# Optimization experiments

Hardware: AMD Instinct MI355X
Metric: run time of the kernel (lower is better)

## Reference

```python
import jax, jax.numpy as jnp
import numpy as np

B, D, M = 1024, 4096, 128          # batch, input_dim, output_dim (num modules)
HS = [32, 64, 128, 256, 512]       # hidden_dims


def setup_inputs() -> dict:
    key = jax.random.key(0)
    ks = jax.random.split(key, 12)
    inp = {}
    inp["x"] = jax.random.normal(ks[0], (B, D), dtype=jnp.float32)
    # first dense layer: Linear(input_dim, hidden_dims[0]*output_dim)
    inp["W0"] = jax.random.normal(ks[1], (HS[0] * M, D), dtype=jnp.float32) / np.float32(np.sqrt(D))
    inp["b0"] = jnp.zeros((HS[0] * M,), jnp.float32)
    # block-diagonal MaskedLinear layers stored as per-module blocks [M, h_out, h_in]
    for i in range(len(HS) - 1):
        inp[f"W{i+1}"] = jax.random.normal(ks[2 + i], (M, HS[i + 1], HS[i]), dtype=jnp.float32) / np.float32(np.sqrt(HS[i]))
        inp[f"b{i+1}"] = jnp.zeros((M, HS[i + 1]), jnp.float32)
    # output MaskedLinear(h_last, 1, M): blocks [M, 1, h_last] stored as [M, h_last]
    inp["Wout"] = jax.random.normal(ks[10], (M, HS[-1]), dtype=jnp.float32) / np.float32(np.sqrt(HS[-1]))
    inp["bout"] = jnp.zeros((M,), jnp.float32)
    return inp


def reference(x, W0, b0, W1, b1, W2, b2, W3, b3, W4, b4, Wout, bout):
    # Dropout is inference-disabled; MaskedLinear's block-diagonal dense GEMM is
    # computed exactly as a grouped GEMM over the M module blocks (same math,
    # skipping the structurally-zero off-diagonal blocks).
    h = jax.nn.relu(x @ W0.T + b0)                 # [B, M*h0]
    h = h.reshape(x.shape[0], M, HS[0])            # [B, M, h0]
    for W, b in ((W1, b1), (W2, b2), (W3, b3), (W4, b4)):
        h = jax.nn.relu(jnp.einsum('bmi,moi->bmo', h, W) + b)  # [B, M, h_out]
    logits = jnp.einsum('bmi,mi->bm', h, Wout) + bout          # [B, M]
    return jax.nn.sigmoid(logits)
```

## Files before the change

### kernel.cpp

```cpp
#include <hip/hip_runtime.h>
#include <hip/hip_bf16.h>


using bf16 = __hip_bfloat16;
typedef short bf16x8 __attribute__((ext_vector_type(8)));
typedef float f32x4 __attribute__((ext_vector_type(4)));

constexpr int B_ = 1024;
constexpr int M_ = 128;

__device__ __forceinline__ void gload16_lds(const bf16* gp, bf16* lp) {
    __builtin_amdgcn_global_load_lds(
        (__attribute__((address_space(1))) void*)const_cast<bf16*>(gp),
        (__attribute__((address_space(3))) void*)lp,
        16, 0, 0);
}

struct CvtArgs {
    const float4* src[6];
    short4* dst[6];
};
__global__ void cvt_all(CvtArgs a) {
    constexpr int starts[7] = {0, 1048576, 5242880, 5308416, 5570560,
                               6619136, 10813440};
    int i = blockIdx.x * blockDim.x + threadIdx.x;
    if (i >= starts[6]) return;
    int s = 0;
#pragma unroll
    for (int k = 1; k < 6; ++k) s += (i >= starts[k]) ? 1 : 0;
    int off = i - starts[s];
    float4 v = a.src[s][off];
    union { bf16 h[4]; short4 s4; } u;
    u.h[0] = __float2bfloat16(v.x);
    u.h[1] = __float2bfloat16(v.y);
    u.h[2] = __float2bfloat16(v.z);
    u.h[3] = __float2bfloat16(v.w);
    a.dst[s][off] = u.s4;
}

template<int BM, int BN>
__global__ __launch_bounds__(256)
void gemm_bt_relu(const bf16* __restrict__ A, int lda,
                  const bf16* __restrict__ W,
                  const float* __restrict__ bias,
                  bf16* __restrict__ C, int ldc,
                  int K) {
    constexpr int BK = 32;
    constexpr int WM = BM / 2, WN = BN / 2;
    constexpr int TM = WM / 16, TN = WN / 16;
    constexpr int A_W = BM / 64;
    constexpr int B_W = BN / 64;

    __shared__ __align__(16) bf16 sA[BM][BK];
    __shared__ __align__(16) bf16 sB[BN][BK];

    const int tid = threadIdx.x;
    const int wid = tid >> 6;
    const int lane = tid & 63;
    const int wm = wid >> 1, wn = wid & 1;
    const int q = lane >> 4, ln = lane & 15;
    const int lr = lane >> 2, lk = lane & 3;

    const int r0 = blockIdx.y * BM;
    const int c0 = blockIdx.x * BN;

    const bf16* gA[A_W];
    bf16* lA[A_W];
#pragma unroll
    for (int t = 0; t < A_W; ++t) {
        int grp = wid * A_W + t;
        gA[t] = A + (size_t)(r0 + grp * 16 + lr) * lda + lk * 8;
        lA[t] = &sA[grp * 16][0];
    }
    const bf16* gB[B_W];
    bf16* lB[B_W];
#pragma unroll
    for (int t = 0; t < B_W; ++t) {
        int grp = wid * B_W + t;
        gB[t] = W + (size_t)(c0 + grp * 16 + lr) * K + lk * 8;
        lB[t] = &sB[grp * 16][0];
    }

    f32x4 acc[TM][TN];
#pragma unroll
    for (int i = 0; i < TM; ++i)
#pragma unroll
        for (int j = 0; j < TN; ++j)
            acc[i][j] = (f32x4){0.f, 0.f, 0.f, 0.f};

    for (int k0 = 0; k0 < K; k0 += BK) {
#pragma unroll
        for (int t = 0; t < A_W; ++t) gload16_lds(gA[t] + k0, lA[t]);
#pragma unroll
        for (int t = 0; t < B_W; ++t) gload16_lds(gB[t] + k0, lB[t]);
        __syncthreads();

        bf16x8 aF[TM], bF[TN];
#pragma unroll
        for (int i = 0; i < TM; ++i)
            aF[i] = *(const bf16x8*)&sA[wm * WM + i * 16 + ln][q * 8];
#pragma unroll
        for (int j = 0; j < TN; ++j)
            bF[j] = *(const bf16x8*)&sB[wn * WN + j * 16 + ln][q * 8];
#pragma unroll
        for (int i = 0; i < TM; ++i)
#pragma unroll
            for (int j = 0; j < TN; ++j)
                acc[i][j] = __builtin_amdgcn_mfma_f32_16x16x32_bf16(aF[i], bF[j], acc[i][j], 0, 0, 0);
        __syncthreads();
    }

#pragma unroll
    for (int j = 0; j < TN; ++j) {
        int col = c0 + wn * WN + j * 16 + ln;
        float bv = bias[col];
#pragma unroll
        for (int i = 0; i < TM; ++i) {
#pragma unroll
            for (int r = 0; r < 4; ++r) {
                int row = r0 + wm * WM + i * 16 + q * 4 + r;
                float v = acc[i][j][r] + bv;
                v = v > 0.f ? v : 0.f;
                C[(size_t)row * ldc + col] = __float2bfloat16(v);
            }
        }
    }
}

__global__ __launch_bounds__(256)
void modules_fused(const bf16* __restrict__ h0g,
                   const bf16* __restrict__ W1b, const float* __restrict__ b1,
                   const bf16* __restrict__ W2b, const float* __restrict__ b2,
                   const bf16* __restrict__ W3b, const float* __restrict__ b3,
                   const bf16* __restrict__ W4b, const float* __restrict__ b4,
                   const float* __restrict__ Wout, const float* __restrict__ bout,
                   float* __restrict__ out) {
    constexpr int H3O = 0, H2O = 16384, H1O = 24576, H0O = 28672;
    constexpr int W1O = 30720, W2O = 28672, W3O = 24576, W4O = 16384;
    __shared__ __align__(16) bf16 pool[32768];

    const int tid = threadIdx.x, w = tid >> 6, lane = tid & 63;
    const int q = lane >> 4, ln = lane & 15;
    const int lr = lane >> 2, lk = lane & 3;
    const int swz = (lk ^ (lr & 3)) * 8;
    const int m = blockIdx.y;
    const int r0 = blockIdx.x * 64;

    const bf16* W1m = W1b + (size_t)m * 64 * 32;
    const bf16* W2m = W2b + (size_t)m * 128 * 64;
    const bf16* W3m = W3b + (size_t)m * 256 * 128;
    const bf16* W4m = W4b + (size_t)m * 512 * 256;

    auto stageW = [&](const bf16* G, int ldg, int rows, int nr0, int k0, int woff) {
        for (int t = 0; t < rows / 64; ++t) {
            int r = t * 64 + w * 16 + lr;
            gload16_lds(G + (size_t)(nr0 + r) * ldg + k0 + swz,
                        pool + woff + t * 2048 + w * 512);
        }
    };
    auto readA = [&](int hoff, int C, int row, int kc) -> bf16x8 {
        return *(const bf16x8*)&pool[hoff + row * (C * 8) + ((kc ^ (row & (C - 1))) * 8)];
    };
    auto readB = [&](int woff, int rn) -> bf16x8 {
        return *(const bf16x8*)&pool[woff + rn * 32 + ((q ^ (rn & 3)) * 8)];
    };
    auto writeH = [&](int hoff, int C, int row, int col, float v) {
        pool[hoff + row * (C * 8) + (((col >> 3) ^ (row & (C - 1))) * 8) + (col & 7)] =
            __float2bfloat16(v);
    };

    gload16_lds(h0g + (size_t)(r0 + w * 16 + lr) * 4096 + m * 32 + swz,
                pool + H0O + w * 512);
    stageW(W1m, 32, 64, 0, 0, W1O);
    __syncthreads();
    {
        f32x4 a1[4];
#pragma unroll
        for (int i = 0; i < 4; ++i) a1[i] = (f32x4){0.f, 0.f, 0.f, 0.f};
        bf16x8 bfr = readB(W1O, w * 16 + ln);
#pragma unroll
        for (int i = 0; i < 4; ++i) {
            bf16x8 af = readA(H0O, 4, i * 16 + ln, q);
            a1[i] = __builtin_amdgcn_mfma_f32_16x16x32_bf16(af, bfr, a1[i], 0, 0, 0);
        }
        int col = w * 16 + ln;
        float bb = b1[m * 64 + col];
#pragma unroll
        for (int i = 0; i < 4; ++i)
#pragma unroll
            for (int r = 0; r < 4; ++r) {
                float v = a1[i][r] + bb;
                v = v > 0.f ? v : 0.f;
                writeH(H1O, 8, i * 16 + q * 4 + r, col, v);
            }
    }
    __syncthreads();

    {
        f32x4 a2[4][2];
#pragma unroll
        for (int i = 0; i < 4; ++i)
#pragma unroll
            for (int j = 0; j < 2; ++j) a2[i][j] = (f32x4){0.f, 0.f, 0.f, 0.f};
#pragma unroll
        for (int kr = 0; kr < 2; ++kr) {
            stageW(W2m, 64, 128, 0, kr * 32, W2O);
            __syncthreads();
            bf16x8 bfr[2];
#pragma unroll
            for (int j = 0; j < 2; ++j) bfr[j] = readB(W2O, w * 32 + j * 16 + ln);
#pragma unroll
            for (int i = 0; i < 4; ++i) {
                bf16x8 af = readA(H1O, 8, i * 16 + ln, kr * 4 + q);
#pragma unroll
                for (int j = 0; j < 2; ++j)
                    a2[i][j] = __builtin_amdgcn_mfma_f32_16x16x32_bf16(af, bfr[j], a2[i][j], 0, 0, 0);
            }
            __syncthreads();
        }
#pragma unroll
        for (int j = 0; j < 2; ++j) {
            int col = w * 32 + j * 16 + ln;
            float bb = b2[m * 128 + col];
#pragma unroll
            for (int i = 0; i < 4; ++i)
#pragma unroll
                for (int r = 0; r < 4; ++r) {
                    float v = a2[i][j][r] + bb;
                    v = v > 0.f ? v : 0.f;
                    writeH(H2O, 16, i * 16 + q * 4 + r, col, v);
                }
        }
    }
    __syncthreads();

    {
        f32x4 a3[4][4];
#pragma unroll
        for (int i = 0; i < 4; ++i)
#pragma unroll
            for (int j = 0; j < 4; ++j) a3[i][j] = (f32x4){0.f, 0.f, 0.f, 0.f};
#pragma unroll
        for (int kr = 0; kr < 4; ++kr) {
            stageW(W3m, 128, 256, 0, kr * 32, W3O);
            __syncthreads();
            bf16x8 bfr[4];
#pragma unroll
            for (int j = 0; j < 4; ++j) bfr[j] = readB(W3O, w * 64 + j * 16 + ln);
#pragma unroll
            for (int i = 0; i < 4; ++i) {
                bf16x8 af = readA(H2O, 16, i * 16 + ln, kr * 4 + q);
#pragma unroll
                for (int j = 0; j < 4; ++j)
                    a3[i][j] = __builtin_amdgcn_mfma_f32_16x16x32_bf16(af, bfr[j], a3[i][j], 0, 0, 0);
            }
            __syncthreads();
        }
#pragma unroll
        for (int j = 0; j < 4; ++j) {
            int col = w * 64 + j * 16 + ln;
            float bb = b3[m * 256 + col];
#pragma unroll
            for (int i = 0; i < 4; ++i)
#pragma unroll
                for (int r = 0; r < 4; ++r) {
                    float v = a3[i][j][r] + bb;
                    v = v > 0.f ? v : 0.f;
                    writeH(H3O, 32, i * 16 + q * 4 + r, col, v);
                }
        }
    }
    __syncthreads();

    float pl[4][4];
#pragma unroll
    for (int i = 0; i < 4; ++i)
#pragma unroll
        for (int r = 0; r < 4; ++r) pl[i][r] = 0.f;

#pragma unroll
    for (int nc = 0; nc < 2; ++nc) {
        f32x4 a4[4][4];
#pragma unroll
        for (int i = 0; i < 4; ++i)
#pragma unroll
            for (int j = 0; j < 4; ++j) a4[i][j] = (f32x4){0.f, 0.f, 0.f, 0.f};
#pragma unroll
        for (int kr = 0; kr < 8; ++kr) {
            stageW(W4m, 256, 256, nc * 256, kr * 32, W4O);
            __syncthreads();
            bf16x8 bfr[4];
#pragma unroll
            for (int j = 0; j < 4; ++j) bfr[j] = readB(W4O, w * 64 + j * 16 + ln);
#pragma unroll
            for (int i = 0; i < 4; ++i) {
                bf16x8 af = readA(H3O, 32, i * 16 + ln, kr * 4 + q);
#pragma unroll
                for (int j = 0; j < 4; ++j)
                    a4[i][j] = __builtin_amdgcn_mfma_f32_16x16x32_bf16(af, bfr[j], a4[i][j], 0, 0, 0);
            }
            __syncthreads();
        }
#pragma unroll
        for (int j = 0; j < 4; ++j) {
            int col = nc * 256 + w * 64 + j * 16 + ln;
            float bb = b4[m * 512 + col];
            float wv = Wout[m * 512 + col];
#pragma unroll
            for (int i = 0; i < 4; ++i)
#pragma unroll
                for (int r = 0; r < 4; ++r) {
                    float v = a4[i][j][r] + bb;
                    v = v > 0.f ? v : 0.f;
                    pl[i][r] += v * wv;
                }
        }
    }

    float* sc = (float*)&pool[W4O];
#pragma unroll
    for (int i = 0; i < 4; ++i)
#pragma unroll
        for (int r = 0; r < 4; ++r) {
            float p = pl[i][r];
            p += __shfl_xor(p, 1);
            p += __shfl_xor(p, 2);
            p += __shfl_xor(p, 4);
            p += __shfl_xor(p, 8);
            if (ln == 0) sc[w * 64 + i * 16 + q * 4 + r] = p;
        }
    __syncthreads();
    if (tid < 64) {
        float s = sc[tid] + sc[64 + tid] + sc[128 + tid] + sc[192 + tid];
        float lg = s + bout[m];
        out[(size_t)(r0 + tid) * M_ + m] = 1.f / (1.f + __expf(-lg));
    }
}

extern "C" void kernel_launch(void* const* d_in, const int* in_sizes, int n_in,
                              void* d_out, int out_size, void* d_ws, size_t ws_size,
                              hipStream_t stream) {
    const float* x    = (const float*)d_in[0];
    const float* W0   = (const float*)d_in[1];
    const float* b0   = (const float*)d_in[2];
    const float* W1   = (const float*)d_in[3];
    const float* b1   = (const float*)d_in[4];
    const float* W2   = (const float*)d_in[5];
    const float* b2   = (const float*)d_in[6];
    const float* W3   = (const float*)d_in[7];
    const float* b3   = (const float*)d_in[8];
    const float* W4   = (const float*)d_in[9];
    const float* b4   = (const float*)d_in[10];
    const float* Wout = (const float*)d_in[11];
    const float* bout = (const float*)d_in[12];
    float* out = (float*)d_out;

    char* ws = (char*)d_ws;
    size_t off = 0;
    auto alloc = [&](size_t bytes) -> void* {
        off = (off + 255) & ~(size_t)255;
        void* p = ws + off;
        off += bytes;
        return p;
    };
    bf16* W0b = (bf16*)alloc((size_t)4096 * 4096 * 2);
    bf16* W1b = (bf16*)alloc((size_t)M_ * 64 * 32 * 2);
    bf16* W2b = (bf16*)alloc((size_t)M_ * 128 * 64 * 2);
    bf16* W3b = (bf16*)alloc((size_t)M_ * 256 * 128 * 2);
    bf16* W4b = (bf16*)alloc((size_t)M_ * 512 * 256 * 2);
    bf16* xb  = (bf16*)alloc((size_t)B_ * 4096 * 2);
    bf16* h0  = (bf16*)alloc((size_t)B_ * 4096 * 2);

    CvtArgs ca;
    ca.src[0] = (const float4*)x;  ca.dst[0] = (short4*)xb;
    ca.src[1] = (const float4*)W0; ca.dst[1] = (short4*)W0b;
    ca.src[2] = (const float4*)W1; ca.dst[2] = (short4*)W1b;
    ca.src[3] = (const float4*)W2; ca.dst[3] = (short4*)W2b;
    ca.src[4] = (const float4*)W3; ca.dst[4] = (short4*)W3b;
    ca.src[5] = (const float4*)W4; ca.dst[5] = (short4*)W4b;
    cvt_all<<<(10813440 + 255) / 256, 256, 0, stream>>>(ca);

    {
        dim3 g(4096 / 64, B_ / 128, 1);
        gemm_bt_relu<128, 64><<<g, 256, 0, stream>>>(xb, 4096, W0b, b0, h0, 4096, 4096);
    }
    {
        dim3 g(B_ / 64, M_, 1);
        modules_fused<<<g, 256, 0, stream>>>(h0, W1b, b1, W2b, b2, W3b, b3,
                                             W4b, b4, Wout, bout, out);
    }
}
```

Baseline: 356.7 us.

## Software-pipeline both GEMM kernels with multi-buffered async LDS loads

Replaces the generic layer-0 GEMM with a specialized kernel that double-buffers K=64 chunks, uses XOR-swizzled LDS layout, and overlaps global->LDS loads with MFMA using explicit vmcnt waits and barriers. The fused module kernel is likewise restructured: weight tiles for the next layer are prefetched during the current layer, layer 4 uses a triple-buffered 128-column pipeline, activations switch to padded row strides instead of XOR swizzles, and biases/Wout are preloaded into registers. The goal is to hide global load latency that the earlier load-sync-compute loops exposed. Hand-counted waitcnt values and occupancy hints of 2 blocks per CU add correctness and register-pressure risk.

```diff
diff --git a/kernel.cpp b/kernel.cpp
--- a/kernel.cpp
+++ b/kernel.cpp
@@ -8,6 +8,10 @@
 
 constexpr int B_ = 1024;
 constexpr int M_ = 128;
+
+#define WAITV(N) asm volatile("s_waitcnt vmcnt(" #N ")" ::: "memory")
+#define WAITL()  asm volatile("s_waitcnt lgkmcnt(0)" ::: "memory")
+#define BAR()    asm volatile("s_barrier" ::: "memory")
 
 __device__ __forceinline__ void gload16_lds(const bf16* gp, bf16* lp) {
     __builtin_amdgcn_global_load_lds(
@@ -38,96 +42,91 @@
     a.dst[s][off] = u.s4;
 }
 
-template<int BM, int BN>
-__global__ __launch_bounds__(256)
-void gemm_bt_relu(const bf16* __restrict__ A, int lda,
-                  const bf16* __restrict__ W,
-                  const float* __restrict__ bias,
-                  bf16* __restrict__ C, int ldc,
-                  int K) {
-    constexpr int BK = 32;
-    constexpr int WM = BM / 2, WN = BN / 2;
-    constexpr int TM = WM / 16, TN = WN / 16;
-    constexpr int A_W = BM / 64;
-    constexpr int B_W = BN / 64;
-
-    __shared__ __align__(16) bf16 sA[BM][BK];
-    __shared__ __align__(16) bf16 sB[BN][BK];
-
-    const int tid = threadIdx.x;
-    const int wid = tid >> 6;
-    const int lane = tid & 63;
-    const int wm = wid >> 1, wn = wid & 1;
+__global__ __launch_bounds__(256, 2)
+void gemm_l0(const bf16* __restrict__ A, const bf16* __restrict__ W,
+             const float* __restrict__ bias, bf16* __restrict__ C) {
+    constexpr int LDA = 4096;
+    __shared__ __align__(16) bf16 sA[2][2][128 * 32];
+    __shared__ __align__(16) bf16 sB[2][2][64 * 32];
+
+    const int tid = threadIdx.x, w = tid >> 6, lane = tid & 63;
     const int q = lane >> 4, ln = lane & 15;
     const int lr = lane >> 2, lk = lane & 3;
-
-    const int r0 = blockIdx.y * BM;
-    const int c0 = blockIdx.x * BN;
-
-    const bf16* gA[A_W];
-    bf16* lA[A_W];
-#pragma unroll
-    for (int t = 0; t < A_W; ++t) {
-        int grp = wid * A_W + t;
-        gA[t] = A + (size_t)(r0 + grp * 16 + lr) * lda + lk * 8;
-        lA[t] = &sA[grp * 16][0];
-    }
-    const bf16* gB[B_W];
-    bf16* lB[B_W];
-#pragma unroll
-    for (int t = 0; t < B_W; ++t) {
-        int grp = wid * B_W + t;
-        gB[t] = W + (size_t)(c0 + grp * 16 + lr) * K + lk * 8;
-        lB[t] = &sB[grp * 16][0];
-    }
-
-    f32x4 acc[TM][TN];
-#pragma unroll
-    for (int i = 0; i < TM; ++i)
-#pragma unroll
-        for (int j = 0; j < TN; ++j)
-            acc[i][j] = (f32x4){0.f, 0.f, 0.f, 0.f};
-
-    for (int k0 = 0; k0 < K; k0 += BK) {
-#pragma unroll
-        for (int t = 0; t < A_W; ++t) gload16_lds(gA[t] + k0, lA[t]);
-#pragma unroll
-        for (int t = 0; t < B_W; ++t) gload16_lds(gB[t] + k0, lB[t]);
-        __syncthreads();
-
-        bf16x8 aF[TM], bF[TN];
-#pragma unroll
-        for (int i = 0; i < TM; ++i)
-            aF[i] = *(const bf16x8*)&sA[wm * WM + i * 16 + ln][q * 8];
-#pragma unroll
-        for (int j = 0; j < TN; ++j)
-            bF[j] = *(const bf16x8*)&sB[wn * WN + j * 16 + ln][q * 8];
-#pragma unroll
-        for (int i = 0; i < TM; ++i)
-#pragma unroll
-            for (int j = 0; j < TN; ++j)
-                acc[i][j] = __builtin_amdgcn_mfma_f32_16x16x32_bf16(aF[i], bF[j], acc[i][j], 0, 0, 0);
-        __syncthreads();
-    }
-
-#pragma unroll
-    for (int j = 0; j < TN; ++j) {
-        int col = c0 + wn * WN + j * 16 + ln;
+    const int swz = (lk ^ (lr & 3)) * 8;
+    const int wm = w >> 1, wn = w & 1;
+    const int r0 = blockIdx.y * 128, c0 = blockIdx.x * 64;
+
+    auto stage = [&](int s, int set) {
+        const int k0 = s * 64;
+#pragma unroll
+        for (int h = 0; h < 2; ++h) {
+#pragma unroll
+            for (int t = 0; t < 2; ++t) {
+                int grp = w * 2 + t;
+                gload16_lds(A + (size_t)(r0 + grp * 16 + lr) * LDA + k0 + h * 32 + swz,
+                            &sA[set][h][grp * 512]);
+            }
+            gload16_lds(W + (size_t)(c0 + w * 16 + lr) * LDA + k0 + h * 32 + swz,
+                        &sB[set][h][w * 512]);
+        }
+    };
+
+    f32x4 acc[4][2];
+#pragma unroll
+    for (int i = 0; i < 4; ++i)
+#pragma unroll
+        for (int j = 0; j < 2; ++j) acc[i][j] = (f32x4){0.f, 0.f, 0.f, 0.f};
+
+    stage(0, 0);
+    stage(1, 1);
+    for (int r = 0; r < 64; ++r) {
+        if (r < 63) WAITV(6); else WAITV(0);
+        BAR();
+        const int set = r & 1;
+        bf16x8 aF[2][4], bF[2][2];
+#pragma unroll
+        for (int h = 0; h < 2; ++h) {
+#pragma unroll
+            for (int i = 0; i < 4; ++i) {
+                int row = wm * 64 + i * 16 + ln;
+                aF[h][i] = *(const bf16x8*)&sA[set][h][row * 32 + ((q ^ (row & 3)) * 8)];
+            }
+#pragma unroll
+            for (int j = 0; j < 2; ++j) {
+                int rn = wn * 32 + j * 16 + ln;
+                bF[h][j] = *(const bf16x8*)&sB[set][h][rn * 32 + ((q ^ (rn & 3)) * 8)];
+            }
+        }
+        WAITL();
+        BAR();
+        if (r + 2 < 64) stage(r + 2, set);
+#pragma unroll
+        for (int h = 0; h < 2; ++h)
+#pragma unroll
+            for (int i = 0; i < 4; ++i)
+#pragma unroll
+                for (int j = 0; j < 2; ++j)
+                    acc[i][j] = __builtin_amdgcn_mfma_f32_16x16x32_bf16(
+                        aF[h][i], bF[h][j], acc[i][j], 0, 0, 0);
+    }
+
+#pragma unroll
+    for (int j = 0; j < 2; ++j) {
+        int col = c0 + wn * 32 + j * 16 + ln;
         float bv = bias[col];
 #pragma unroll
-        for (int i = 0; i < TM; ++i) {
-#pragma unroll
-            for (int r = 0; r < 4; ++r) {
-                int row = r0 + wm * WM + i * 16 + q * 4 + r;
-                float v = acc[i][j][r] + bv;
+        for (int i = 0; i < 4; ++i)
+#pragma unroll
+            for (int rr = 0; rr < 4; ++rr) {
+                int row = r0 + wm * 64 + i * 16 + q * 4 + rr;
+                float v = acc[i][j][rr] + bv;
                 v = v > 0.f ? v : 0.f;
-                C[(size_t)row * ldc + col] = __float2bfloat16(v);
-            }
-        }
+                C[(size_t)row * 4096 + col] = __float2bfloat16(v);
+            }
     }
 }
 
-__global__ __launch_bounds__(256)
+__global__ __launch_bounds__(256, 2)
 void modules_fused(const bf16* __restrict__ h0g,
                    const bf16* __restrict__ W1b, const float* __restrict__ b1,
                    const bf16* __restrict__ W2b, const float* __restrict__ b2,
@@ -135,8 +134,8 @@
                    const bf16* __restrict__ W4b, const float* __restrict__ b4,
                    const float* __restrict__ Wout, const float* __restrict__ bout,
                    float* __restrict__ out) {
-    constexpr int H3O = 0, H2O = 16384, H1O = 24576, H0O = 28672;
-    constexpr int W1O = 30720, W2O = 28672, W3O = 24576, W4O = 16384;
+    constexpr int H3O = 0, H2O = 16896, H1O = 25600, H0O = 30208;
+    constexpr int P4B0 = 16896, P4B1 = 20992, P4B2 = 25600;
     __shared__ __align__(16) bf16 pool[32768];
 
     const int tid = threadIdx.x, w = tid >> 6, lane = tid & 63;
@@ -151,50 +150,77 @@
     const bf16* W3m = W3b + (size_t)m * 256 * 128;
     const bf16* W4m = W4b + (size_t)m * 512 * 256;
 
-    auto stageW = [&](const bf16* G, int ldg, int rows, int nr0, int k0, int woff) {
+    auto stage = [&](const bf16* G, int ldg, int rows, int nr0, int k0, int woff) {
+#pragma unroll
         for (int t = 0; t < rows / 64; ++t) {
             int r = t * 64 + w * 16 + lr;
             gload16_lds(G + (size_t)(nr0 + r) * ldg + k0 + swz,
                         pool + woff + t * 2048 + w * 512);
         }
     };
-    auto readA = [&](int hoff, int C, int row, int kc) -> bf16x8 {
-        return *(const bf16x8*)&pool[hoff + row * (C * 8) + ((kc ^ (row & (C - 1))) * 8)];
-    };
-    auto readB = [&](int woff, int rn) -> bf16x8 {
+    auto rdA = [&](int hoff, int stride, int row, int kc) -> bf16x8 {
+        return *(const bf16x8*)&pool[hoff + row * stride + kc * 8];
+    };
+    auto rdA0 = [&](int row) -> bf16x8 {
+        return *(const bf16x8*)&pool[H0O + row * 32 + ((q ^ (row & 3)) * 8)];
+    };
+    auto rdB = [&](int woff, int rn) -> bf16x8 {
         return *(const bf16x8*)&pool[woff + rn * 32 + ((q ^ (rn & 3)) * 8)];
     };
-    auto writeH = [&](int hoff, int C, int row, int col, float v) {
-        pool[hoff + row * (C * 8) + (((col >> 3) ^ (row & (C - 1))) * 8) + (col & 7)] =
-            __float2bfloat16(v);
-    };
+    auto wrH = [&](int hoff, int stride, int row, int col, float v) {
+        pool[hoff + row * stride + col] = __float2bfloat16(v);
+    };
+
+    float b1v = b1[m * 64 + w * 16 + ln];
+    float b2v[2], b3v[4], b4v[4][2], wov[4][2];
+#pragma unroll
+    for (int j = 0; j < 2; ++j) b2v[j] = b2[m * 128 + w * 32 + j * 16 + ln];
+#pragma unroll
+    for (int j = 0; j < 4; ++j) b3v[j] = b3[m * 256 + w * 64 + j * 16 + ln];
+#pragma unroll
+    for (int nc = 0; nc < 4; ++nc)
+#pragma unroll
+        for (int j = 0; j < 2; ++j) {
+            int col = nc * 128 + w * 32 + j * 16 + ln;
+            b4v[nc][j] = b4[(size_t)m * 512 + col];
+            wov[nc][j] = Wout[(size_t)m * 512 + col];
+        }
+    float boutv = bout[m];
+    WAITV(0);
 
     gload16_lds(h0g + (size_t)(r0 + w * 16 + lr) * 4096 + m * 32 + swz,
                 pool + H0O + w * 512);
-    stageW(W1m, 32, 64, 0, 0, W1O);
-    __syncthreads();
+    stage(W1m, 32, 64, 0, 0, 8192);
+    stage(W2m, 64, 128, 0, 0, 0);
+    stage(W2m, 64, 128, 0, 32, 4096);
+
+    WAITV(4);
+    BAR();
     {
+        bf16x8 aF[4], bF;
+#pragma unroll
+        for (int i = 0; i < 4; ++i) aF[i] = rdA0(i * 16 + ln);
+        bF = rdB(8192, w * 16 + ln);
+        WAITL();
+        BAR();
         f32x4 a1[4];
 #pragma unroll
-        for (int i = 0; i < 4; ++i) a1[i] = (f32x4){0.f, 0.f, 0.f, 0.f};
-        bf16x8 bfr = readB(W1O, w * 16 + ln);
-#pragma unroll
         for (int i = 0; i < 4; ++i) {
-            bf16x8 af = readA(H0O, 4, i * 16 + ln, q);
-            a1[i] = __builtin_amdgcn_mfma_f32_16x16x32_bf16(af, bfr, a1[i], 0, 0, 0);
+            a1[i] = (f32x4){0.f, 0.f, 0.f, 0.f};
+            a1[i] = __builtin_amdgcn_mfma_f32_16x16x32_bf16(aF[i], bF, a1[i], 0, 0, 0);
         }
         int col = w * 16 + ln;
-        float bb = b1[m * 64 + col];
 #pragma unroll
         for (int i = 0; i < 4; ++i)
 #pragma unroll
-            for (int r = 0; r < 4; ++r) {
-                float v = a1[i][r] + bb;
+            for (int rr = 0; rr < 4; ++rr) {
+                float v = a1[i][rr] + b1v;
                 v = v > 0.f ? v : 0.f;
-                writeH(H1O, 8, i * 16 + q * 4 + r, col, v);
-            }
-    }
-    __syncthreads();
+                wrH(H1O, 72, i * 16 + q * 4 + rr, col, v);
+            }
+        WAITL();
+        BAR();
+    }
 
     {
         f32x4 a2[4][2];
@@ -204,35 +230,40 @@
             for (int j = 0; j < 2; ++j) a2[i][j] = (f32x4){0.f, 0.f, 0.f, 0.f};
 #pragma unroll
         for (int kr = 0; kr < 2; ++kr) {
-            stageW(W2m, 64, 128, 0, kr * 32, W2O);
-            __syncthreads();
-            bf16x8 bfr[2];
-#pragma unroll
-            for (int j = 0; j < 2; ++j) bfr[j] = readB(W2O, w * 32 + j * 16 + ln);
-#pragma unroll
-            for (int i = 0; i < 4; ++i) {
-                bf16x8 af = readA(H1O, 8, i * 16 + ln, kr * 4 + q);
+            if (kr == 0) WAITV(2); else WAITV(0);
+            BAR();
+            bf16x8 aF[4], bF[2];
+#pragma unroll
+            for (int i = 0; i < 4; ++i) aF[i] = rdA(H1O, 72, i * 16 + ln, kr * 4 + q);
+#pragma unroll
+            for (int j = 0; j < 2; ++j) bF[j] = rdB(kr * 4096, w * 32 + j * 16 + ln);
+            WAITL();
+            BAR();
+            if (kr == 1) {
+                stage(W3m, 128, 256, 0, 0, 0);
+                stage(W3m, 128, 256, 0, 32, 8192);
+            }
+#pragma unroll
+            for (int i = 0; i < 4; ++i)
 #pragma unroll
                 for (int j = 0; j < 2; ++j)
-                    a2[i][j] = __builtin_amdgcn_mfma_f32_16x16x32_bf16(af, bfr[j], a2[i][j], 0, 0, 0);
-            }
-            __syncthreads();
+                    a2[i][j] = __builtin_amdgcn_mfma_f32_16x16x32_bf16(aF[i], bF[j], a2[i][j], 0, 0, 0);
         }
 #pragma unroll
         for (int j = 0; j < 2; ++j) {
             int col = w * 32 + j * 16 + ln;
-            float bb = b2[m * 128 + col];
-#pragma unroll
-            for (int i = 0; i < 4; ++i)
-#pragma unroll
-                for (int r = 0; r < 4; ++r) {
-                    float v = a2[i][j][r] + bb;
+#pragma unroll
+            for (int i = 0; i < 4; ++i)
+#pragma unroll
+                for (int rr = 0; rr < 4; ++rr) {
+                    float v = a2[i][j][rr] + b2v[j];
                     v = v > 0.f ? v : 0.f;
-                    writeH(H2O, 16, i * 16 + q * 4 + r, col, v);
+                    wrH(H2O, 136, i * 16 + q * 4 + rr, col, v);
                 }
         }
-    }
-    __syncthreads();
+        WAITL();
+        BAR();
+    }
 
     {
         f32x4 a3[4][4];
@@ -242,97 +273,110 @@
             for (int j = 0; j < 4; ++j) a3[i][j] = (f32x4){0.f, 0.f, 0.f, 0.f};
 #pragma unroll
         for (int kr = 0; kr < 4; ++kr) {
-            stageW(W3m, 128, 256, 0, kr * 32, W3O);
-            __syncthreads();
-            bf16x8 bfr[4];
-#pragma unroll
-            for (int j = 0; j < 4; ++j) bfr[j] = readB(W3O, w * 64 + j * 16 + ln);
-#pragma unroll
-            for (int i = 0; i < 4; ++i) {
-                bf16x8 af = readA(H2O, 16, i * 16 + ln, kr * 4 + q);
+            if (kr < 3) WAITV(4); else WAITV(0);
+            BAR();
+            bf16x8 aF[4], bF[4];
+#pragma unroll
+            for (int i = 0; i < 4; ++i) aF[i] = rdA(H2O, 136, i * 16 + ln, kr * 4 + q);
+#pragma unroll
+            for (int j = 0; j < 4; ++j) bF[j] = rdB((kr & 1) * 8192, w * 64 + j * 16 + ln);
+            WAITL();
+            BAR();
+            if (kr == 0)      stage(W3m, 128, 256, 0, 64, 0);
+            else if (kr == 1) stage(W3m, 128, 256, 0, 96, 8192);
+            else if (kr == 3) {
+                stage(W4m, 256, 128, 0, 0, P4B0);
+                stage(W4m, 256, 128, 0, 32, P4B1);
+            }
+#pragma unroll
+            for (int i = 0; i < 4; ++i)
 #pragma unroll
                 for (int j = 0; j < 4; ++j)
-                    a3[i][j] = __builtin_amdgcn_mfma_f32_16x16x32_bf16(af, bfr[j], a3[i][j], 0, 0, 0);
-            }
-            __syncthreads();
+                    a3[i][j] = __builtin_amdgcn_mfma_f32_16x16x32_bf16(aF[i], bF[j], a3[i][j], 0, 0, 0);
         }
 #pragma unroll
         for (int j = 0; j < 4; ++j) {
             int col = w * 64 + j * 16 + ln;
-            float bb = b3[m * 256 + col];
-#pragma unroll
-            for (int i = 0; i < 4; ++i)
-#pragma unroll
-                for (int r = 0; r < 4; ++r) {
-                    float v = a3[i][j][r] + bb;
+#pragma unroll
+            for (int i = 0; i < 4; ++i)
+#pragma unroll
+                for (int rr = 0; rr < 4; ++rr) {
+                    float v = a3[i][j][rr] + b3v[j];
                     v = v > 0.f ? v : 0.f;
-                    writeH(H3O, 32, i * 16 + q * 4 + r, col, v);
+                    wrH(H3O, 264, i * 16 + q * 4 + rr, col, v);
                 }
         }
-    }
-    __syncthreads();
+        WAITL();
+        BAR();
+    }
 
     float pl[4][4];
 #pragma unroll
     for (int i = 0; i < 4; ++i)
 #pragma unroll
-        for (int r = 0; r < 4; ++r) pl[i][r] = 0.f;
-
-#pragma unroll
-    for (int nc = 0; nc < 2; ++nc) {
-        f32x4 a4[4][4];
+        for (int rr = 0; rr < 4; ++rr) pl[i][rr] = 0.f;
+
+#pragma unroll
+    for (int nc = 0; nc < 4; ++nc) {
+        f32x4 a4[4][2];
 #pragma unroll
         for (int i = 0; i < 4; ++i)
 #pragma unroll
-            for (int j = 0; j < 4; ++j) a4[i][j] = (f32x4){0.f, 0.f, 0.f, 0.f};
+            for (int j = 0; j < 2; ++j) a4[i][j] = (f32x4){0.f, 0.f, 0.f, 0.f};
 #pragma unroll
         for (int kr = 0; kr < 8; ++kr) {
-            stageW(W4m, 256, 256, nc * 256, kr * 32, W4O);
-            __syncthreads();
-            bf16x8 bfr[4];
-#pragma unroll
-            for (int j = 0; j < 4; ++j) bfr[j] = readB(W4O, w * 64 + j * 16 + ln);
-#pragma unroll
-            for (int i = 0; i < 4; ++i) {
-                bf16x8 af = readA(H3O, 32, i * 16 + ln, kr * 4 + q);
-#pragma unroll
-                for (int j = 0; j < 4; ++j)
-                    a4[i][j] = __builtin_amdgcn_mfma_f32_16x16x32_bf16(af, bfr[j], a4[i][j], 0, 0, 0);
-            }
-            __syncthreads();
-        }
-#pragma unroll
-        for (int j = 0; j < 4; ++j) {
-            int col = nc * 256 + w * 64 + j * 16 + ln;
-            float bb = b4[m * 512 + col];
-            float wv = Wout[m * 512 + col];
-#pragma unroll
-            for (int i = 0; i < 4; ++i)
-#pragma unroll
-                for (int r = 0; r < 4; ++r) {
-                    float v = a4[i][j][r] + bb;
+            const int r = nc * 8 + kr;
+            if (r + 2 < 32) {
+                const int r2 = r + 2;
+                const int wb2 = (r2 % 3 == 0) ? P4B0 : (r2 % 3 == 1) ? P4B1 : P4B2;
+                stage(W4m, 256, 128, (r2 >> 3) * 128, (r2 & 7) * 32, wb2);
+            }
+            if (r < 30) WAITV(4); else if (r == 30) WAITV(2); else WAITV(0);
+            BAR();
+            const int wb = (r % 3 == 0) ? P4B0 : (r % 3 == 1) ? P4B1 : P4B2;
+            bf16x8 aF[4], bF[2];
+#pragma unroll
+            for (int i = 0; i < 4; ++i) aF[i] = rdA(H3O, 264, i * 16 + ln, kr * 4 + q);
+#pragma unroll
+            for (int j = 0; j < 2; ++j) bF[j] = rdB(wb, w * 32 + j * 16 + ln);
+            WAITL();
+            BAR();
+#pragma unroll
+            for (int i = 0; i < 4; ++i)
+#pragma unroll
+                for (int j = 0; j < 2; ++j)
+                    a4[i][j] = __builtin_amdgcn_mfma_f32_16x16x32_bf16(aF[i], bF[j], a4[i][j], 0, 0, 0);
+        }
+#pragma unroll
+        for (int j = 0; j < 2; ++j) {
+            float bb = b4v[nc][j], wv = wov[nc][j];
+#pragma unroll
+            for (int i = 0; i < 4; ++i)
+#pragma unroll
+                for (int rr = 0; rr < 4; ++rr) {
+                    float v = a4[i][j][rr] + bb;
                     v = v > 0.f ? v : 0.f;
-                    pl[i][r] += v * wv;
+                    pl[i][rr] += v * wv;
                 }
         }
     }
 
-    float* sc = (float*)&pool[W4O];
+    float* sc = (float*)&pool[H0O];
 #pragma unroll
     for (int i = 0; i < 4; ++i)
 #pragma unroll
-        for (int r = 0; r < 4; ++r) {
-            float p = pl[i][r];
+        for (int rr = 0; rr < 4; ++rr) {
+            float p = pl[i][rr];
             p += __shfl_xor(p, 1);
             p += __shfl_xor(p, 2);
             p += __shfl_xor(p, 4);
             p += __shfl_xor(p, 8);
-            if (ln == 0) sc[w * 64 + i * 16 + q * 4 + r] = p;
+            if (ln == 0) sc[w * 64 + i * 16 + q * 4 + rr] = p;
         }
     __syncthreads();
     if (tid < 64) {
         float s = sc[tid] + sc[64 + tid] + sc[128 + tid] + sc[192 + tid];
-        float lg = s + bout[m];
+        float lg = s + boutv;
         out[(size_t)(r0 + tid) * M_ + m] = 1.f / (1.f + __expf(-lg));
     }
 }
@@ -382,7 +426,7 @@
 
     {
         dim3 g(4096 / 64, B_ / 128, 1);
-        gemm_bt_relu<128, 64><<<g, 256, 0, stream>>>(xb, 4096, W0b, b0, h0, 4096, 4096);
+        gemm_l0<<<g, 256, 0, stream>>>(xb, W0b, b0, h0);
     }
     {
         dim3 g(B_ / 64, M_, 1);
```

Result: faster. 323.8 us (-9.2%).
